# Optimization experiments

Measured on AMD Instinct MI355X. Metric: run time of the kernel, lower is better.

Reference implementation:

```python
import jax, jax.numpy as jnp
import numpy as np

BATCH = 65536
SEQ_LEN = 32
EMB = 64
H = 128


def setup_inputs() -> dict:
    key = jax.random.key(0)
    ks = jax.random.split(key, 12)
    s = 0.05
    inp = {
        "last_pos": jax.random.normal(ks[0], (BATCH, 2), jnp.float32),
        "last_pos_rel": jax.random.normal(ks[1], (BATCH, 2), jnp.float32),
        "hh": jax.random.normal(ks[2], (1, BATCH, H), jnp.float32),
        "ch": jax.random.normal(ks[3], (1, BATCH, H), jnp.float32),
        "seq_start_end": jnp.sort(jax.random.randint(ks[4], (256, 2), 0, BATCH), axis=0),
        # LSTM(embedding_dim -> h_dim), PyTorch gate order [i, f, g, o]
        "w_ih": jax.random.normal(ks[5], (4 * H, EMB), jnp.float32) * s,
        "w_hh": jax.random.normal(ks[6], (4 * H, H), jnp.float32) * s,
        "b_ih": jax.random.normal(ks[7], (4 * H,), jnp.float32) * s,
        "b_hh": jax.random.normal(ks[8], (4 * H,), jnp.float32) * s,
        # spatial_embedding: Linear(2 -> EMB)
        "w_emb": jax.random.normal(ks[9], (EMB, 2), jnp.float32) * s,
        "b_emb": jax.random.normal(ks[10], (EMB,), jnp.float32) * s,
        # hidden2pos: Linear(H -> 2)
        "w_pos": jax.random.normal(ks[11], (2, H), jnp.float32) * s,
        "b_pos": jnp.zeros((2,), jnp.float32),
    }
    return inp


def _decode(last_pos, last_pos_rel, hh, ch, w_ih, w_hh, b_ih, b_hh,
            w_emb, b_emb, w_pos, b_pos):
    h0, c0 = hh[0], ch[0]                      # (B, H)
    x0 = last_pos_rel @ w_emb.T + b_emb        # (B, EMB)
    b = b_ih + b_hh

    def step(carry, _):
        h, c, lp, x = carry
        gates = x @ w_ih.T + h @ w_hh.T + b    # (B, 4H)
        i, f, g, o = jnp.split(gates, 4, axis=-1)
        c2 = jax.nn.sigmoid(f) * c + jax.nn.sigmoid(i) * jnp.tanh(g)
        h2 = jax.nn.sigmoid(o) * jnp.tanh(c2)
        rel = h2 @ w_pos.T + b_pos             # (B, 2)
        cur = rel + lp
        x2 = rel @ w_emb.T + b_emb             # next decoder input embedding
        return (h2, c2, cur, x2), rel

    (hN, cN, _, _), rels = jax.lax.scan(step, (h0, c0, last_pos, x0),
                                        None, length=SEQ_LEN)
    # rels: (SEQ_LEN, B, 2) == pred_traj_fake_rel; hN[None]: (1, B, H)
    return rels, hN[None]


def reference(last_pos, last_pos_rel, hh, ch, seq_start_end,
              w_ih, w_hh, b_ih, b_hh, w_emb, b_emb, w_pos, b_pos):
    # seq_start_end is unused when pool_every_timestep=False
    return _decode(last_pos, last_pos_rel, hh, ch,
                   w_ih, w_hh, b_ih, b_hh, w_emb, b_emb, w_pos, b_pos)
```

## Files before the change

### kernel.cpp

```cpp
#include <hip/hip_runtime.h>

#define B_TOT 65536
#define SEQ   32

typedef __bf16 bf16_8 __attribute__((ext_vector_type(8)));
typedef __bf16 bf16_4 __attribute__((ext_vector_type(4)));
typedef float  float4v __attribute__((ext_vector_type(4)));
typedef float  float2v __attribute__((ext_vector_type(2)));

#define SC1 (-1.4426950408889634f)
#define SC2 (-2.8853900817779268f)

__device__ inline unsigned short f2bf(float f){
    unsigned u = __builtin_bit_cast(unsigned, f);
    u += 0x7FFFu + ((u >> 16) & 1u);
    return (unsigned short)(u >> 16);
}

__device__ inline float2v v_exp2(float2v x){
    float2v r; r[0] = __builtin_amdgcn_exp2f(x[0]); r[1] = __builtin_amdgcn_exp2f(x[1]); return r;
}
__device__ inline float2v v_rcp(float2v x){
    float2v r; r[0] = __builtin_amdgcn_rcpf(x[0]); r[1] = __builtin_amdgcn_rcpf(x[1]); return r;
}
__device__ inline float2v v_fma(float2v a, float2v b, float2v c){
    float2v r; r[0] = __builtin_fmaf(a[0], b[0], c[0]); r[1] = __builtin_fmaf(a[1], b[1], c[1]); return r;
}

__global__ void prep_kernel(const float* __restrict__ w_ih,
                            const float* __restrict__ w_hh,
                            const float* __restrict__ b_ih,
                            const float* __restrict__ b_hh,
                            const float* __restrict__ w_emb,
                            const float* __restrict__ b_emb,
                            const float* __restrict__ w_pos,
                            const float* __restrict__ b_pos,
                            unsigned short* __restrict__ weff,
                            float* __restrict__ beff,
                            float* __restrict__ m2,
                            unsigned short* __restrict__ wposA)
{
    int n = threadIdx.x;
    float m20 = 0.f, m21 = 0.f, bi = 0.f;
    for (int e = 0; e < 64; ++e){
        float wv = w_ih[n*64 + e];
        m20 += w_emb[e*2 + 0] * wv;
        m21 += w_emb[e*2 + 1] * wv;
        bi  += b_emb[e] * wv;
    }
    float sc = ((n >> 7) == 2) ? SC2 : SC1;
    m2[n]       = m20 * sc;
    m2[512 + n] = m21 * sc;
    beff[n] = (b_ih[n] + b_hh[n] + bi + b_pos[0]*m20 + b_pos[1]*m21) * sc;
    for (int k = 0; k < 128; ++k){
        float wv = w_hh[n*128 + k] + w_pos[k]*m20 + w_pos[128 + k]*m21;
        weff[n*128 + k] = f2bf(wv * sc);
    }
    if (n < 256) wposA[n] = f2bf(w_pos[n]);
    for (int idx = n; idx < 14*128; idx += 512) wposA[256 + idx] = 0;
}

__global__ __launch_bounds__(256, 2) void dec_kernel(
    const float* __restrict__ lpr,
    const float* __restrict__ hh,
    const float* __restrict__ ch,
    const float* __restrict__ b_pos,
    const unsigned short* __restrict__ wposA,
    const unsigned short* __restrict__ weff,
    const float* __restrict__ beff,
    const float* __restrict__ m2,
    float* __restrict__ out)
{
    __shared__ __align__(16) unsigned short lh[2][16][152];
    __shared__ float ubuf[16][2];
    __shared__ __align__(16) float hsh[16][132];

    const int tid  = threadIdx.x;
    const int w    = tid >> 6;
    const int lane = tid & 63;
    const int q    = lane >> 4;
    const int l    = lane & 15;
    const int row0 = blockIdx.x << 4;
    const int batch = row0 + l;

    const float2v one2 = {1.f, 1.f};
    const float2v sc22 = {SC2, SC2};

    bf16_8 wA[8][4];
    float4v bias4[8];
#pragma unroll
    for (int t8 = 0; t8 < 8; ++t8){
        int nbase = ((t8 >> 1) << 7) + 32*w + ((t8 & 1) << 4);
        int gA = nbase + l;
#pragma unroll
        for (int kt = 0; kt < 4; ++kt)
            wA[t8][kt] = *(const bf16_8*)(weff + (gA << 7) + kt*32 + (q << 3));
        bias4[t8] = *(const float4v*)(beff + nbase + (q << 2));
    }

    bf16_8 wpA[4];
#pragma unroll
    for (int kt = 0; kt < 4; ++kt)
        wpA[kt] = *(const bf16_8*)(wposA + (l << 7) + kt*32 + (q << 3));
    const float bp0 = b_pos[0], bp1 = b_pos[1];

    float2v cstp[2][2];
#pragma unroll
    for (int X = 0; X < 2; ++X){
        float4v cv = *(const float4v*)(ch + (batch << 7) + 32*w + 16*X + (q << 2));
        float2v clo = {cv[0], cv[1]};
        float2v chi = {cv[2], cv[3]};
        cstp[X][0] = clo;
        cstp[X][1] = chi;
    }

    bf16_8 b[4];
#pragma unroll
    for (int kt = 0; kt < 4; ++kt){
        const float* ph = hh + (batch << 7) + kt*32 + (q << 3);
        float4v h0 = *(const float4v*)ph;
        float4v h1 = *(const float4v*)(ph + 4);
        bf16_8 t;
        t[0]=(__bf16)h0[0]; t[1]=(__bf16)h0[1]; t[2]=(__bf16)h0[2]; t[3]=(__bf16)h0[3];
        t[4]=(__bf16)h1[0]; t[5]=(__bf16)h1[1]; t[6]=(__bf16)h1[2]; t[7]=(__bf16)h1[3];
        b[kt] = t;
    }

    if (w == 0){
        float4v r = {0.f, 0.f, 0.f, 0.f};
#pragma unroll
        for (int kt = 0; kt < 4; ++kt)
            r = __builtin_amdgcn_mfma_f32_16x16x32_bf16(wpA[kt], b[kt], r, 0, 0, 0);
        if (q == 0){
            float2v lp = *(const float2v*)(lpr + (batch << 1));
            ubuf[l][0] = lp[0] - (r[0] + bp0);
            ubuf[l][1] = lp[1] - (r[1] + bp1);
        }
    }
    __syncthreads();

    float4v acc[8];

    auto do_gates = [&](){
#pragma unroll
        for (int t8 = 0; t8 < 8; ++t8)
            acc[t8] = __builtin_amdgcn_mfma_f32_16x16x32_bf16(wA[t8][0], b[0], bias4[t8], 0, 0, 0);
#pragma unroll
        for (int kt = 1; kt < 4; ++kt)
#pragma unroll
            for (int t8 = 0; t8 < 8; ++t8)
                acc[t8] = __builtin_amdgcn_mfma_f32_16x16x32_bf16(wA[t8][kt], b[kt], acc[t8], 0, 0, 0);
    };

    auto do_elem_write = [&](int buf, bool finalh){
#pragma unroll
        for (int X = 0; X < 2; ++X){
            bf16_4 hv;
#pragma unroll
            for (int p = 0; p < 2; ++p){
                float2v iv = {acc[0 + X][2*p], acc[0 + X][2*p + 1]};
                float2v fv = {acc[2 + X][2*p], acc[2 + X][2*p + 1]};
                float2v gv = {acc[4 + X][2*p], acc[4 + X][2*p + 1]};
                float2v ov = {acc[6 + X][2*p], acc[6 + X][2*p + 1]};
                float2v ei = v_exp2(iv);
                float2v ef = v_exp2(fv);
                float2v eg = v_exp2(gv);
                float2v pi_ = ei + one2;
                float2v pf  = ef + one2;
                float2v pg  = eg + one2;
                float2v mg  = one2 - eg;
                float2v t2  = pi_ * pg;
                float2v den = pf * t2;
                float2v num = v_fma(cstp[X][p], t2, pf * mg);
                float2v c2  = num * v_rcp(den);
                float2v eo  = v_exp2(ov);
                float2v ec  = v_exp2(c2 * sc22);
                float2v po  = eo + one2;
                float2v pc  = ec + one2;
                float2v mc  = one2 - ec;
                float2v h2  = mc * v_rcp(po * pc);
                cstp[X][p] = c2;
                hv[2*p]     = (__bf16)h2[0];
                hv[2*p + 1] = (__bf16)h2[1];
                if (finalh){
                    int cb = 32*w + 16*X + (q << 2) + 2*p;
                    hsh[l][cb]     = h2[0];
                    hsh[l][cb + 1] = h2[1];
                }
            }
            *(bf16_4*)&lh[buf][l][32*w + 16*X + (q << 2)] = hv;
        }
    };

    auto reload_and_rel = [&](int buf, int t){
#pragma unroll
        for (int kt = 0; kt < 4; ++kt)
            b[kt] = *(const bf16_8*)&lh[buf][l][kt*32 + (q << 3)];
        if (w == (t & 3)){
            float4v r = {0.f, 0.f, 0.f, 0.f};
#pragma unroll
            for (int kt = 0; kt < 4; ++kt)
                r = __builtin_amdgcn_mfma_f32_16x16x32_bf16(wpA[kt], b[kt], r, 0, 0, 0);
            if (q == 0){
                float2v rv;
                rv[0] = r[0] + bp0;
                rv[1] = r[1] + bp1;
                *(float2v*)(out + t*(B_TOT*2) + (batch << 1)) = rv;
            }
        }
    };

    do_gates();
    {
        float u0 = ubuf[l][0], u1 = ubuf[l][1];
#pragma unroll
        for (int t8 = 0; t8 < 8; ++t8){
            int g0 = ((t8 >> 1) << 7) + 32*w + ((t8 & 1) << 4) + (q << 2);
            float4v ma = *(const float4v*)(m2 + g0);
            float4v mb = *(const float4v*)(m2 + 512 + g0);
#pragma unroll
            for (int r4 = 0; r4 < 4; ++r4)
                acc[t8][r4] += u0*ma[r4] + u1*mb[r4];
        }
    }
    do_elem_write(1, false);
    __syncthreads();
    reload_and_rel(1, 0);

    for (int t = 1; t < SEQ; ++t){
        do_gates();
        do_elem_write((t + 1) & 1, t == SEQ - 1);
        __syncthreads();
        reload_and_rel((t + 1) & 1, t);
    }

    __syncthreads();
    {
        int r = tid >> 4, c8 = (tid & 15) << 3;
        float4v v0 = *(const float4v*)&hsh[r][c8];
        float4v v1 = *(const float4v*)&hsh[r][c8 + 4];
        float* po = out + SEQ*B_TOT*2 + ((row0 + r) << 7) + c8;
        *(float4v*)po = v0;
        *(float4v*)(po + 4) = v1;
    }
}

extern "C" void kernel_launch(void* const* d_in, const int* in_sizes, int n_in,
                              void* d_out, int out_size, void* d_ws, size_t ws_size,
                              hipStream_t stream)
{
    (void)in_sizes; (void)n_in; (void)out_size; (void)ws_size;

    const float* lpr   = (const float*)d_in[1];
    const float* hh    = (const float*)d_in[2];
    const float* ch    = (const float*)d_in[3];
    const float* w_ih  = (const float*)d_in[5];
    const float* w_hh  = (const float*)d_in[6];
    const float* b_ih  = (const float*)d_in[7];
    const float* b_hh  = (const float*)d_in[8];
    const float* w_emb = (const float*)d_in[9];
    const float* b_emb = (const float*)d_in[10];
    const float* w_pos = (const float*)d_in[11];
    const float* b_pos = (const float*)d_in[12];

    unsigned short* weff  = (unsigned short*)d_ws;
    float* beff           = (float*)((char*)d_ws + 131072);
    float* m2             = (float*)((char*)d_ws + 131072 + 2048);
    unsigned short* wposA = (unsigned short*)((char*)d_ws + 131072 + 2048 + 4096);

    hipLaunchKernelGGL(prep_kernel, dim3(1), dim3(512), 0, stream,
                       w_ih, w_hh, b_ih, b_hh, w_emb, b_emb, w_pos, b_pos,
                       weff, beff, m2, wposA);
    hipLaunchKernelGGL(dec_kernel, dim3(B_TOT/16), dim3(256), 0, stream,
                       lpr, hh, ch, b_pos, wposA, weff, beff, m2,
                       (float*)d_out);
}
```

Measured before the change: 489.7 us.

## Interleave two 16-row batch tiles per block to overlap MFMA with elementwise

Each block now handles 32 batch rows as two independent 16-row tiles, A and B. It software-pipelines them so the gate MFMAs of one tile are issued alongside the elementwise LSTM update of the other. The aim is to hide the MFMA latency and the barrier stalls of the serial recurrence, and to amortize the register-resident weights over twice as many rows. The cost is a doubled register footprint: launch bounds drop to one block per SIMD pair, the grid is halved, and occupancy falls.

New measurement: 602.3 us. 23.0% more time.

```diff
diff --git a/kernel.cpp b/kernel.cpp
--- a/kernel.cpp
+++ b/kernel.cpp
@@ -60,7 +60,7 @@
     for (int idx = n; idx < 14*128; idx += 512) wposA[256 + idx] = 0;
 }
 
-__global__ __launch_bounds__(256, 2) void dec_kernel(
+__global__ __launch_bounds__(256, 1) void dec_kernel(
     const float* __restrict__ lpr,
     const float* __restrict__ hh,
     const float* __restrict__ ch,
@@ -71,17 +71,19 @@
     const float* __restrict__ m2,
     float* __restrict__ out)
 {
-    __shared__ __align__(16) unsigned short lh[2][16][152];
-    __shared__ float ubuf[16][2];
-    __shared__ __align__(16) float hsh[16][132];
+    __shared__ __align__(16) unsigned short lhA[16][152];
+    __shared__ __align__(16) unsigned short lhB[16][152];
+    __shared__ float ubuf[32][2];
+    __shared__ __align__(16) float hsh[32][132];
 
     const int tid  = threadIdx.x;
     const int w    = tid >> 6;
     const int lane = tid & 63;
     const int q    = lane >> 4;
     const int l    = lane & 15;
-    const int row0 = blockIdx.x << 4;
-    const int batch = row0 + l;
+    const int row0 = blockIdx.x << 5;
+    const int batchA = row0 + l;
+    const int batchB = row0 + 16 + l;
 
     const float2v one2 = {1.f, 1.f};
     const float2v sc22 = {SC2, SC2};
@@ -104,44 +106,61 @@
         wpA[kt] = *(const bf16_8*)(wposA + (l << 7) + kt*32 + (q << 3));
     const float bp0 = b_pos[0], bp1 = b_pos[1];
 
-    float2v cstp[2][2];
+    float2v cstA[2][2], cstB[2][2];
 #pragma unroll
     for (int X = 0; X < 2; ++X){
-        float4v cv = *(const float4v*)(ch + (batch << 7) + 32*w + 16*X + (q << 2));
-        float2v clo = {cv[0], cv[1]};
-        float2v chi = {cv[2], cv[3]};
-        cstp[X][0] = clo;
-        cstp[X][1] = chi;
-    }
-
-    bf16_8 b[4];
+        float4v ca = *(const float4v*)(ch + (batchA << 7) + 32*w + 16*X + (q << 2));
+        float4v cb = *(const float4v*)(ch + (batchB << 7) + 32*w + 16*X + (q << 2));
+        float2v t;
+        t[0]=ca[0]; t[1]=ca[1]; cstA[X][0]=t;
+        t[0]=ca[2]; t[1]=ca[3]; cstA[X][1]=t;
+        t[0]=cb[0]; t[1]=cb[1]; cstB[X][0]=t;
+        t[0]=cb[2]; t[1]=cb[3]; cstB[X][1]=t;
+    }
+
+    bf16_8 bA[4], bB[4];
 #pragma unroll
     for (int kt = 0; kt < 4; ++kt){
-        const float* ph = hh + (batch << 7) + kt*32 + (q << 3);
-        float4v h0 = *(const float4v*)ph;
-        float4v h1 = *(const float4v*)(ph + 4);
-        bf16_8 t;
-        t[0]=(__bf16)h0[0]; t[1]=(__bf16)h0[1]; t[2]=(__bf16)h0[2]; t[3]=(__bf16)h0[3];
-        t[4]=(__bf16)h1[0]; t[5]=(__bf16)h1[1]; t[6]=(__bf16)h1[2]; t[7]=(__bf16)h1[3];
-        b[kt] = t;
+        const float* pa = hh + (batchA << 7) + kt*32 + (q << 3);
+        const float* pb = hh + (batchB << 7) + kt*32 + (q << 3);
+        float4v a0 = *(const float4v*)pa;      float4v a1 = *(const float4v*)(pa + 4);
+        float4v c0 = *(const float4v*)pb;      float4v c1 = *(const float4v*)(pb + 4);
+        bf16_8 ta, tb;
+        ta[0]=(__bf16)a0[0]; ta[1]=(__bf16)a0[1]; ta[2]=(__bf16)a0[2]; ta[3]=(__bf16)a0[3];
+        ta[4]=(__bf16)a1[0]; ta[5]=(__bf16)a1[1]; ta[6]=(__bf16)a1[2]; ta[7]=(__bf16)a1[3];
+        tb[0]=(__bf16)c0[0]; tb[1]=(__bf16)c0[1]; tb[2]=(__bf16)c0[2]; tb[3]=(__bf16)c0[3];
+        tb[4]=(__bf16)c1[0]; tb[5]=(__bf16)c1[1]; tb[6]=(__bf16)c1[2]; tb[7]=(__bf16)c1[3];
+        bA[kt] = ta;
+        bB[kt] = tb;
     }
 
     if (w == 0){
         float4v r = {0.f, 0.f, 0.f, 0.f};
 #pragma unroll
         for (int kt = 0; kt < 4; ++kt)
-            r = __builtin_amdgcn_mfma_f32_16x16x32_bf16(wpA[kt], b[kt], r, 0, 0, 0);
+            r = __builtin_amdgcn_mfma_f32_16x16x32_bf16(wpA[kt], bA[kt], r, 0, 0, 0);
         if (q == 0){
-            float2v lp = *(const float2v*)(lpr + (batch << 1));
+            float2v lp = *(const float2v*)(lpr + (batchA << 1));
             ubuf[l][0] = lp[0] - (r[0] + bp0);
             ubuf[l][1] = lp[1] - (r[1] + bp1);
         }
     }
+    if (w == 1){
+        float4v r = {0.f, 0.f, 0.f, 0.f};
+#pragma unroll
+        for (int kt = 0; kt < 4; ++kt)
+            r = __builtin_amdgcn_mfma_f32_16x16x32_bf16(wpA[kt], bB[kt], r, 0, 0, 0);
+        if (q == 0){
+            float2v lp = *(const float2v*)(lpr + (batchB << 1));
+            ubuf[16 + l][0] = lp[0] - (r[0] + bp0);
+            ubuf[16 + l][1] = lp[1] - (r[1] + bp1);
+        }
+    }
     __syncthreads();
 
-    float4v acc[8];
-
-    auto do_gates = [&](){
+    float4v accA[8], accB[8];
+
+    auto do_gates = [&](float4v (&acc)[8], bf16_8 (&b)[4]){
 #pragma unroll
         for (int t8 = 0; t8 < 8; ++t8)
             acc[t8] = __builtin_amdgcn_mfma_f32_16x16x32_bf16(wA[t8][0], b[0], bias4[t8], 0, 0, 0);
@@ -152,7 +171,21 @@
                 acc[t8] = __builtin_amdgcn_mfma_f32_16x16x32_bf16(wA[t8][kt], b[kt], acc[t8], 0, 0, 0);
     };
 
-    auto do_elem_write = [&](int buf, bool finalh){
+    auto u0fix = [&](float4v (&acc)[8], int ur){
+        float u0 = ubuf[ur][0], u1 = ubuf[ur][1];
+#pragma unroll
+        for (int t8 = 0; t8 < 8; ++t8){
+            int g0 = ((t8 >> 1) << 7) + 32*w + ((t8 & 1) << 4) + (q << 2);
+            float4v ma = *(const float4v*)(m2 + g0);
+            float4v mb = *(const float4v*)(m2 + 512 + g0);
+#pragma unroll
+            for (int r4 = 0; r4 < 4; ++r4)
+                acc[t8][r4] += u0*ma[r4] + u1*mb[r4];
+        }
+    };
+
+    auto elem_write = [&](float4v (&acc)[8], float2v (&cst)[2][2],
+                          unsigned short (*lhp)[152], bool finalh, int hrow){
 #pragma unroll
         for (int X = 0; X < 2; ++X){
             bf16_4 hv;
@@ -171,7 +204,7 @@
                 float2v mg  = one2 - eg;
                 float2v t2  = pi_ * pg;
                 float2v den = pf * t2;
-                float2v num = v_fma(cstp[X][p], t2, pf * mg);
+                float2v num = v_fma(cst[X][p], t2, pf * mg);
                 float2v c2  = num * v_rcp(den);
                 float2v eo  = v_exp2(ov);
                 float2v ec  = v_exp2(c2 * sc22);
@@ -179,69 +212,67 @@
                 float2v pc  = ec + one2;
                 float2v mc  = one2 - ec;
                 float2v h2  = mc * v_rcp(po * pc);
-                cstp[X][p] = c2;
+                cst[X][p] = c2;
                 hv[2*p]     = (__bf16)h2[0];
                 hv[2*p + 1] = (__bf16)h2[1];
                 if (finalh){
                     int cb = 32*w + 16*X + (q << 2) + 2*p;
-                    hsh[l][cb]     = h2[0];
-                    hsh[l][cb + 1] = h2[1];
+                    hsh[hrow][cb]     = h2[0];
+                    hsh[hrow][cb + 1] = h2[1];
                 }
             }
-            *(bf16_4*)&lh[buf][l][32*w + 16*X + (q << 2)] = hv;
-        }
-    };
-
-    auto reload_and_rel = [&](int buf, int t){
-#pragma unroll
-        for (int kt = 0; kt < 4; ++kt)
-            b[kt] = *(const bf16_8*)&lh[buf][l][kt*32 + (q << 3)];
-        if (w == (t & 3)){
-            float4v r = {0.f, 0.f, 0.f, 0.f};
-#pragma unroll
-            for (int kt = 0; kt < 4; ++kt)
-                r = __builtin_amdgcn_mfma_f32_16x16x32_bf16(wpA[kt], b[kt], r, 0, 0, 0);
-            if (q == 0){
-                float2v rv;
-                rv[0] = r[0] + bp0;
-                rv[1] = r[1] + bp1;
-                *(float2v*)(out + t*(B_TOT*2) + (batch << 1)) = rv;
-            }
-        }
-    };
-
-    do_gates();
-    {
-        float u0 = ubuf[l][0], u1 = ubuf[l][1];
-#pragma unroll
-        for (int t8 = 0; t8 < 8; ++t8){
-            int g0 = ((t8 >> 1) << 7) + 32*w + ((t8 & 1) << 4) + (q << 2);
-            float4v ma = *(const float4v*)(m2 + g0);
-            float4v mb = *(const float4v*)(m2 + 512 + g0);
-#pragma unroll
-            for (int r4 = 0; r4 < 4; ++r4)
-                acc[t8][r4] += u0*ma[r4] + u1*mb[r4];
-        }
-    }
-    do_elem_write(1, false);
-    __syncthreads();
-    reload_and_rel(1, 0);
-
-    for (int t = 1; t < SEQ; ++t){
-        do_gates();
-        do_elem_write((t + 1) & 1, t == SEQ - 1);
+            *(bf16_4*)&lhp[l][32*w + 16*X + (q << 2)] = hv;
+        }
+    };
+
+    auto reload = [&](bf16_8 (&b)[4], const unsigned short (*lhp)[152]){
+#pragma unroll
+        for (int kt = 0; kt < 4; ++kt)
+            b[kt] = *(const bf16_8*)&lhp[l][kt*32 + (q << 3)];
+    };
+
+    auto relout = [&](bf16_8 (&b)[4], int t, int batch){
+        float4v r = {0.f, 0.f, 0.f, 0.f};
+#pragma unroll
+        for (int kt = 0; kt < 4; ++kt)
+            r = __builtin_amdgcn_mfma_f32_16x16x32_bf16(wpA[kt], b[kt], r, 0, 0, 0);
+        if (q == 0){
+            float2v rv;
+            rv[0] = r[0] + bp0;
+            rv[1] = r[1] + bp1;
+            *(float2v*)(out + t*(B_TOT*2) + (batch << 1)) = rv;
+        }
+    };
+
+    do_gates(accA, bA);
+    u0fix(accA, l);
+
+    for (int t = 0; t < SEQ; ++t){
+        do_gates(accB, bB);
+        if (t == 0) u0fix(accB, 16 + l);
+        elem_write(accA, cstA, lhA, t == SEQ - 1, l);
         __syncthreads();
-        reload_and_rel((t + 1) & 1, t);
+        reload(bA, lhA);
+        if (w == (t & 3)) relout(bA, t, batchA);
+        if (t < SEQ - 1) do_gates(accA, bA);
+        elem_write(accB, cstB, lhB, t == SEQ - 1, 16 + l);
+        __syncthreads();
+        reload(bB, lhB);
+        if (w == ((t + 2) & 3)) relout(bB, t, batchB);
     }
 
     __syncthreads();
     {
-        int r = tid >> 4, c8 = (tid & 15) << 3;
-        float4v v0 = *(const float4v*)&hsh[r][c8];
-        float4v v1 = *(const float4v*)&hsh[r][c8 + 4];
-        float* po = out + SEQ*B_TOT*2 + ((row0 + r) << 7) + c8;
+        int r = tid >> 3, c16 = (tid & 7) << 4;
+        float4v v0 = *(const float4v*)&hsh[r][c16];
+        float4v v1 = *(const float4v*)&hsh[r][c16 + 4];
+        float4v v2 = *(const float4v*)&hsh[r][c16 + 8];
+        float4v v3 = *(const float4v*)&hsh[r][c16 + 12];
+        float* po = out + SEQ*B_TOT*2 + ((row0 + r) << 7) + c16;
         *(float4v*)po = v0;
-        *(float4v*)(po + 4) = v1;
+        *(float4v*)(po + 4)  = v1;
+        *(float4v*)(po + 8)  = v2;
+        *(float4v*)(po + 12) = v3;
     }
 }
 
@@ -271,7 +302,7 @@
     hipLaunchKernelGGL(prep_kernel, dim3(1), dim3(512), 0, stream,
                        w_ih, w_hh, b_ih, b_hh, w_emb, b_emb, w_pos, b_pos,
                        weff, beff, m2, wposA);
-    hipLaunchKernelGGL(dec_kernel, dim3(B_TOT/16), dim3(256), 0, stream,
+    hipLaunchKernelGGL(dec_kernel, dim3(B_TOT/32), dim3(256), 0, stream,
                        lpr, hh, ch, b_pos, wposA, weff, beff, m2,
                        (float*)d_out);
 }
```

## Split decoder into producer MFMA waves and consumer elementwise waves over two tiles

Applied to the files above, without the earlier changes.

Each block now holds 32 rows in two 16-row tiles and runs 8 waves. Four producer waves do the gate MFMAs and write the gates to swizzled LDS, while four consumer waves run the sigmoid/tanh cell update for the other tile. The goal is to overlap matrix work with transcendental elementwise work across the two tiles. In exchange it uses about 94KB of dynamic LDS, round-trips gate values through shared memory, and has fewer blocks per CU.

Result: slower. 630.8 us (+28.8%).

```diff
diff --git a/kernel.cpp b/kernel.cpp
--- a/kernel.cpp
+++ b/kernel.cpp
@@ -4,7 +4,6 @@
 #define SEQ   32
 
 typedef __bf16 bf16_8 __attribute__((ext_vector_type(8)));
-typedef __bf16 bf16_4 __attribute__((ext_vector_type(4)));
 typedef float  float4v __attribute__((ext_vector_type(4)));
 typedef float  float2v __attribute__((ext_vector_type(2)));
 
@@ -60,7 +59,7 @@
     for (int idx = n; idx < 14*128; idx += 512) wposA[256 + idx] = 0;
 }
 
-__global__ __launch_bounds__(256, 2) void dec_kernel(
+__global__ __launch_bounds__(512, 2) void dec_kernel(
     const float* __restrict__ lpr,
     const float* __restrict__ hh,
     const float* __restrict__ ch,
@@ -71,174 +70,213 @@
     const float* __restrict__ m2,
     float* __restrict__ out)
 {
-    __shared__ __align__(16) unsigned short lh[2][16][152];
-    __shared__ float ubuf[16][2];
-    __shared__ __align__(16) float hsh[16][132];
+    extern __shared__ __align__(16) char smem[];
+    float* gacc0 = (float*)smem;
+    float* gacc1 = (float*)(smem + 32768);
+    unsigned short* lh0 = (unsigned short*)(smem + 65536);
+    unsigned short* lh1 = (unsigned short*)(smem + 70400);
+    float* ubuf = (float*)(smem + 75264);
+    float* hsh  = (float*)(smem + 75520);
+    float* bsh  = (float*)(smem + 92416);
 
     const int tid  = threadIdx.x;
     const int w    = tid >> 6;
     const int lane = tid & 63;
     const int q    = lane >> 4;
     const int l    = lane & 15;
-    const int row0 = blockIdx.x << 4;
-    const int batch = row0 + l;
+    const int row0 = blockIdx.x << 5;
+    const bool PROD = (w < 4);
 
     const float2v one2 = {1.f, 1.f};
     const float2v sc22 = {SC2, SC2};
 
-    bf16_8 wA[8][4];
-    float4v bias4[8];
-#pragma unroll
-    for (int t8 = 0; t8 < 8; ++t8){
-        int nbase = ((t8 >> 1) << 7) + 32*w + ((t8 & 1) << 4);
-        int gA = nbase + l;
-#pragma unroll
-        for (int kt = 0; kt < 4; ++kt)
-            wA[t8][kt] = *(const bf16_8*)(weff + (gA << 7) + kt*32 + (q << 3));
-        bias4[t8] = *(const float4v*)(beff + nbase + (q << 2));
-    }
-
-    bf16_8 wpA[4];
-#pragma unroll
-    for (int kt = 0; kt < 4; ++kt)
-        wpA[kt] = *(const bf16_8*)(wposA + (l << 7) + kt*32 + (q << 3));
-    const float bp0 = b_pos[0], bp1 = b_pos[1];
-
-    float2v cstp[2][2];
-#pragma unroll
-    for (int X = 0; X < 2; ++X){
-        float4v cv = *(const float4v*)(ch + (batch << 7) + 32*w + 16*X + (q << 2));
-        float2v clo = {cv[0], cv[1]};
-        float2v chi = {cv[2], cv[3]};
-        cstp[X][0] = clo;
-        cstp[X][1] = chi;
-    }
-
-    bf16_8 b[4];
-#pragma unroll
-    for (int kt = 0; kt < 4; ++kt){
-        const float* ph = hh + (batch << 7) + kt*32 + (q << 3);
+    {
+        int X   = tid >> 8;
+        int rid = tid & 255;
+        int il  = rid & 15;
+        int iu0 = (rid >> 4) << 3;
+        const float* ph = hh + ((row0 + (X << 4) + il) << 7) + iu0;
         float4v h0 = *(const float4v*)ph;
         float4v h1 = *(const float4v*)(ph + 4);
         bf16_8 t;
         t[0]=(__bf16)h0[0]; t[1]=(__bf16)h0[1]; t[2]=(__bf16)h0[2]; t[3]=(__bf16)h0[3];
         t[4]=(__bf16)h1[0]; t[5]=(__bf16)h1[1]; t[6]=(__bf16)h1[2]; t[7]=(__bf16)h1[3];
-        b[kt] = t;
-    }
-
-    if (w == 0){
+        unsigned short* lhp = X ? lh1 : lh0;
+        *(bf16_8*)&lhp[il*152 + iu0] = t;
+        bsh[tid] = beff[tid];
+    }
+
+    bf16_8 wA[8][4];
+    bf16_8 wpA[4];
+    float bp0 = 0.f, bp1 = 0.f;
+    float2v cstA[4], cstB[4];
+    int ug = 0, u0 = 0;
+
+    if (PROD){
+#pragma unroll
+        for (int t8 = 0; t8 < 8; ++t8){
+            int nbase = ((t8 >> 1) << 7) + (w << 5) + ((t8 & 1) << 4);
+            int gA = nbase + l;
+#pragma unroll
+            for (int kt = 0; kt < 4; ++kt)
+                wA[t8][kt] = *(const bf16_8*)(weff + (gA << 7) + kt*32 + (q << 3));
+        }
+#pragma unroll
+        for (int kt = 0; kt < 4; ++kt)
+            wpA[kt] = *(const bf16_8*)(wposA + (l << 7) + kt*32 + (q << 3));
+        bp0 = b_pos[0]; bp1 = b_pos[1];
+    } else {
+        int cw = w - 4;
+        ug = (cw << 2) + q;
+        u0 = ug << 3;
+        const float* pca = ch + ((row0 + l) << 7) + u0;
+        const float* pcb = ch + ((row0 + 16 + l) << 7) + u0;
+        float4v ca0 = *(const float4v*)pca;  float4v ca1 = *(const float4v*)(pca + 4);
+        float4v cb0 = *(const float4v*)pcb;  float4v cb1 = *(const float4v*)(pcb + 4);
+        cstA[0][0]=ca0[0]; cstA[0][1]=ca0[1]; cstA[1][0]=ca0[2]; cstA[1][1]=ca0[3];
+        cstA[2][0]=ca1[0]; cstA[2][1]=ca1[1]; cstA[3][0]=ca1[2]; cstA[3][1]=ca1[3];
+        cstB[0][0]=cb0[0]; cstB[0][1]=cb0[1]; cstB[1][0]=cb0[2]; cstB[1][1]=cb0[3];
+        cstB[2][0]=cb1[0]; cstB[2][1]=cb1[1]; cstB[3][0]=cb1[2]; cstB[3][1]=cb1[3];
+    }
+    __syncthreads();
+
+    auto pphase = [&](const unsigned short* lhp, float* gp, int t, int X){
+        bf16_8 b[4];
+#pragma unroll
+        for (int kt = 0; kt < 4; ++kt)
+            b[kt] = *(const bf16_8*)&lhp[l*152 + kt*32 + (q << 3)];
+        float4v a8[8];
+#pragma unroll
+        for (int t8 = 0; t8 < 8; ++t8){
+            int nbase = ((t8 >> 1) << 7) + (w << 5) + ((t8 & 1) << 4);
+            float4v bias4 = *(const float4v*)&bsh[nbase + (q << 2)];
+            a8[t8] = __builtin_amdgcn_mfma_f32_16x16x32_bf16(wA[t8][0], b[0], bias4, 0, 0, 0);
+        }
+#pragma unroll
+        for (int kt = 1; kt < 4; ++kt)
+#pragma unroll
+            for (int t8 = 0; t8 < 8; ++t8)
+                a8[t8] = __builtin_amdgcn_mfma_f32_16x16x32_bf16(wA[t8][kt], b[kt], a8[t8], 0, 0, 0);
+#pragma unroll
+        for (int t8 = 0; t8 < 8; ++t8){
+            int c = ((t8 >> 1) << 5) + (w << 3) + ((t8 & 1) << 2) + q;
+            *(float4v*)&gp[(l << 9) + ((c ^ (l & 7)) << 2)] = a8[t8];
+        }
+        if (w == (t & 3)){
+            float4v r = {0.f, 0.f, 0.f, 0.f};
+#pragma unroll
+            for (int kt = 0; kt < 4; ++kt)
+                r = __builtin_amdgcn_mfma_f32_16x16x32_bf16(wpA[kt], b[kt], r, 0, 0, 0);
+            int batch = row0 + (X << 4) + l;
+            if (t == 0){
+                if (q == 0){
+                    float2v lp = *(const float2v*)(lpr + (batch << 1));
+                    ubuf[(((X << 4) + l) << 1) + 0] = lp[0] - (r[0] + bp0);
+                    ubuf[(((X << 4) + l) << 1) + 1] = lp[1] - (r[1] + bp1);
+                }
+            } else if (q == 0){
+                float2v rv; rv[0] = r[0] + bp0; rv[1] = r[1] + bp1;
+                *(float2v*)(out + (t - 1)*(B_TOT*2) + (batch << 1)) = rv;
+            }
+        }
+    };
+
+    auto prel = [&](const unsigned short* lhp, int X){
+        bf16_8 b[4];
+#pragma unroll
+        for (int kt = 0; kt < 4; ++kt)
+            b[kt] = *(const bf16_8*)&lhp[l*152 + kt*32 + (q << 3)];
         float4v r = {0.f, 0.f, 0.f, 0.f};
 #pragma unroll
         for (int kt = 0; kt < 4; ++kt)
             r = __builtin_amdgcn_mfma_f32_16x16x32_bf16(wpA[kt], b[kt], r, 0, 0, 0);
         if (q == 0){
-            float2v lp = *(const float2v*)(lpr + (batch << 1));
-            ubuf[l][0] = lp[0] - (r[0] + bp0);
-            ubuf[l][1] = lp[1] - (r[1] + bp1);
-        }
+            int batch = row0 + (X << 4) + l;
+            float2v rv; rv[0] = r[0] + bp0; rv[1] = r[1] + bp1;
+            *(float2v*)(out + (SEQ - 1)*(B_TOT*2) + (batch << 1)) = rv;
+        }
+    };
+
+    auto elem = [&](const float* gp, float2v (&cst)[4],
+                    unsigned short* lhp, int X, bool u0f, bool finalh){
+        float4v gv[4][2];
+#pragma unroll
+        for (int g = 0; g < 4; ++g)
+#pragma unroll
+            for (int s = 0; s < 2; ++s){
+                int c = (g << 5) + (ug << 1) + s;
+                gv[g][s] = *(const float4v*)&gp[(l << 9) + ((c ^ (l & 7)) << 2)];
+            }
+        if (u0f){
+            float u0v = ubuf[(((X << 4) + l) << 1) + 0];
+            float u1v = ubuf[(((X << 4) + l) << 1) + 1];
+#pragma unroll
+            for (int g = 0; g < 4; ++g)
+#pragma unroll
+                for (int s = 0; s < 2; ++s){
+                    const float* mp = m2 + (g << 7) + u0 + (s << 2);
+                    float4v ma = *(const float4v*)mp;
+                    float4v mb = *(const float4v*)(mp + 512);
+#pragma unroll
+                    for (int i = 0; i < 4; ++i)
+                        gv[g][s][i] += u0v*ma[i] + u1v*mb[i];
+                }
+        }
+        bf16_8 hv;
+#pragma unroll
+        for (int p = 0; p < 4; ++p){
+            int s = p >> 1, o = (p & 1) << 1;
+            float2v iv = {gv[0][s][o], gv[0][s][o + 1]};
+            float2v fv = {gv[1][s][o], gv[1][s][o + 1]};
+            float2v gz = {gv[2][s][o], gv[2][s][o + 1]};
+            float2v ov = {gv[3][s][o], gv[3][s][o + 1]};
+            float2v ei = v_exp2(iv);
+            float2v ef = v_exp2(fv);
+            float2v eg = v_exp2(gz);
+            float2v pi_ = ei + one2;
+            float2v pf  = ef + one2;
+            float2v pg  = eg + one2;
+            float2v mg  = one2 - eg;
+            float2v t2  = pi_ * pg;
+            float2v den = pf * t2;
+            float2v num = v_fma(cst[p], t2, pf * mg);
+            float2v c2  = num * v_rcp(den);
+            float2v eo  = v_exp2(ov);
+            float2v ec  = v_exp2(c2 * sc22);
+            float2v po  = eo + one2;
+            float2v pc  = ec + one2;
+            float2v mc  = one2 - ec;
+            float2v h2  = mc * v_rcp(po * pc);
+            cst[p] = c2;
+            hv[2*p]     = (__bf16)h2[0];
+            hv[2*p + 1] = (__bf16)h2[1];
+            if (finalh)
+                *(float2v*)&hsh[((X << 4) + l)*132 + u0 + 2*p] = h2;
+        }
+        *(bf16_8*)&lhp[l*152 + u0] = hv;
+    };
+
+    for (int t = 0; t < SEQ; ++t){
+        if (PROD)       pphase(lh0, gacc0, t, 0);
+        else if (t > 0) elem(gacc1, cstB, lh1, 1, t == 1, false);
+        __syncthreads();
+        if (PROD) pphase(lh1, gacc1, t, 1);
+        else      elem(gacc0, cstA, lh0, 0, t == 0, t == SEQ - 1);
+        __syncthreads();
+    }
+    if (PROD){
+        if (w == 0) prel(lh0, 0);
+    } else {
+        elem(gacc1, cstB, lh1, 1, false, true);
     }
     __syncthreads();
-
-    float4v acc[8];
-
-    auto do_gates = [&](){
-#pragma unroll
-        for (int t8 = 0; t8 < 8; ++t8)
-            acc[t8] = __builtin_amdgcn_mfma_f32_16x16x32_bf16(wA[t8][0], b[0], bias4[t8], 0, 0, 0);
-#pragma unroll
-        for (int kt = 1; kt < 4; ++kt)
-#pragma unroll
-            for (int t8 = 0; t8 < 8; ++t8)
-                acc[t8] = __builtin_amdgcn_mfma_f32_16x16x32_bf16(wA[t8][kt], b[kt], acc[t8], 0, 0, 0);
-    };
-
-    auto do_elem_write = [&](int buf, bool finalh){
-#pragma unroll
-        for (int X = 0; X < 2; ++X){
-            bf16_4 hv;
-#pragma unroll
-            for (int p = 0; p < 2; ++p){
-                float2v iv = {acc[0 + X][2*p], acc[0 + X][2*p + 1]};
-                float2v fv = {acc[2 + X][2*p], acc[2 + X][2*p + 1]};
-                float2v gv = {acc[4 + X][2*p], acc[4 + X][2*p + 1]};
-                float2v ov = {acc[6 + X][2*p], acc[6 + X][2*p + 1]};
-                float2v ei = v_exp2(iv);
-                float2v ef = v_exp2(fv);
-                float2v eg = v_exp2(gv);
-                float2v pi_ = ei + one2;
-                float2v pf  = ef + one2;
-                float2v pg  = eg + one2;
-                float2v mg  = one2 - eg;
-                float2v t2  = pi_ * pg;
-                float2v den = pf * t2;
-                float2v num = v_fma(cstp[X][p], t2, pf * mg);
-                float2v c2  = num * v_rcp(den);
-                float2v eo  = v_exp2(ov);
-                float2v ec  = v_exp2(c2 * sc22);
-                float2v po  = eo + one2;
-                float2v pc  = ec + one2;
-                float2v mc  = one2 - ec;
-                float2v h2  = mc * v_rcp(po * pc);
-                cstp[X][p] = c2;
-                hv[2*p]     = (__bf16)h2[0];
-                hv[2*p + 1] = (__bf16)h2[1];
-                if (finalh){
-                    int cb = 32*w + 16*X + (q << 2) + 2*p;
-                    hsh[l][cb]     = h2[0];
-                    hsh[l][cb + 1] = h2[1];
-                }
-            }
-            *(bf16_4*)&lh[buf][l][32*w + 16*X + (q << 2)] = hv;
-        }
-    };
-
-    auto reload_and_rel = [&](int buf, int t){
-#pragma unroll
-        for (int kt = 0; kt < 4; ++kt)
-            b[kt] = *(const bf16_8*)&lh[buf][l][kt*32 + (q << 3)];
-        if (w == (t & 3)){
-            float4v r = {0.f, 0.f, 0.f, 0.f};
-#pragma unroll
-            for (int kt = 0; kt < 4; ++kt)
-                r = __builtin_amdgcn_mfma_f32_16x16x32_bf16(wpA[kt], b[kt], r, 0, 0, 0);
-            if (q == 0){
-                float2v rv;
-                rv[0] = r[0] + bp0;
-                rv[1] = r[1] + bp1;
-                *(float2v*)(out + t*(B_TOT*2) + (batch << 1)) = rv;
-            }
-        }
-    };
-
-    do_gates();
-    {
-        float u0 = ubuf[l][0], u1 = ubuf[l][1];
-#pragma unroll
-        for (int t8 = 0; t8 < 8; ++t8){
-            int g0 = ((t8 >> 1) << 7) + 32*w + ((t8 & 1) << 4) + (q << 2);
-            float4v ma = *(const float4v*)(m2 + g0);
-            float4v mb = *(const float4v*)(m2 + 512 + g0);
-#pragma unroll
-            for (int r4 = 0; r4 < 4; ++r4)
-                acc[t8][r4] += u0*ma[r4] + u1*mb[r4];
-        }
-    }
-    do_elem_write(1, false);
+    if (PROD && w == 1) prel(lh1, 1);
     __syncthreads();
-    reload_and_rel(1, 0);
-
-    for (int t = 1; t < SEQ; ++t){
-        do_gates();
-        do_elem_write((t + 1) & 1, t == SEQ - 1);
-        __syncthreads();
-        reload_and_rel((t + 1) & 1, t);
-    }
-
-    __syncthreads();
+
     {
         int r = tid >> 4, c8 = (tid & 15) << 3;
-        float4v v0 = *(const float4v*)&hsh[r][c8];
-        float4v v1 = *(const float4v*)&hsh[r][c8 + 4];
+        float4v v0 = *(const float4v*)&hsh[r*132 + c8];
+        float4v v1 = *(const float4v*)&hsh[r*132 + c8 + 4];
         float* po = out + SEQ*B_TOT*2 + ((row0 + r) << 7) + c8;
         *(float4v*)po = v0;
         *(float4v*)(po + 4) = v1;
@@ -268,10 +306,18 @@
     float* m2             = (float*)((char*)d_ws + 131072 + 2048);
     unsigned short* wposA = (unsigned short*)((char*)d_ws + 131072 + 2048 + 4096);
 
+    static bool attr_set = false;
+    if (!attr_set){
+        (void)hipFuncSetAttribute((const void*)dec_kernel,
+                                  hipFuncAttributeMaxDynamicSharedMemorySize,
+                                  96*1024);
+        attr_set = true;
+    }
+
     hipLaunchKernelGGL(prep_kernel, dim3(1), dim3(512), 0, stream,
                        w_ih, w_hh, b_ih, b_hh, w_emb, b_emb, w_pos, b_pos,
                        weff, beff, m2, wposA);
-    hipLaunchKernelGGL(dec_kernel, dim3(B_TOT/16), dim3(256), 0, stream,
+    hipLaunchKernelGGL(dec_kernel, dim3(B_TOT/32), dim3(512), 94464, stream,
                        lpr, hh, ch, b_pos, wposA, weff, beff, m2,
                        (float*)d_out);
 }
```
